# Optimization experiments

Hardware: AMD Instinct MI355X
Metric: run time of the kernel (lower is better)

The kernel has to match this reference:

```python
import jax, jax.numpy as jnp
import numpy as np

B_, N, C = 1024, 64, 512
H = 16          # num_heads
NW = 64         # number of windows (B_ % NW == 0)


def setup_inputs() -> dict:
    key = jax.random.key(0)
    ks = jax.random.split(key, 7)
    return {
        "x": jax.random.normal(ks[0], (B_, N, C), jnp.float32),
        "mask": jax.random.normal(ks[1], (NW, N, N), jnp.float32),
        "qkv_w": jax.random.normal(ks[2], (C, 3 * C), jnp.float32) * 0.02,
        "qkv_b": jax.random.normal(ks[3], (3 * C,), jnp.float32) * 0.02,
        "proj_w": jax.random.normal(ks[4], (C, C), jnp.float32) * 0.02,
        "proj_b": jax.random.normal(ks[5], (C,), jnp.float32) * 0.02,
        "bias_table": jax.random.normal(ks[6], (2 * N - 1, H), jnp.float32) * 0.02,
    }


def reference(x, mask, qkv_w, qkv_b, proj_w, proj_b, bias_table):
    b_, n, c = x.shape
    h = bias_table.shape[1]
    ws = (bias_table.shape[0] + 1) // 2  # window_size, == n here
    d = c // h
    scale = d ** -0.5

    qkv = x @ qkv_w + qkv_b                                   # [B_, N, 3C]
    qkv = qkv.reshape(b_, n, 3, h, d).transpose(2, 0, 3, 1, 4)  # [3, B_, H, N, d]
    q, k, v = qkv[0] * scale, qkv[1], qkv[2]

    attn = jnp.einsum('bhnd,bhmd->bhnm', q, k)                # [B_, H, N, N]

    coords = jnp.arange(ws)
    rel_idx = coords[:, None] - coords[None, :] + ws - 1       # [ws, ws]
    bias = bias_table[rel_idx].transpose(2, 0, 1)              # [H, ws, ws]
    attn = attn + bias[None]

    nw = mask.shape[0]
    attn = attn.reshape(b_ // nw, nw, h, n, n) + mask[None, :, None]
    attn = attn.reshape(-1, h, n, n)
    attn = jax.nn.softmax(attn, axis=-1)

    out = jnp.einsum('bhnm,bhmd->bhnd', attn, v)               # [B_, H, N, d]
    # Faithful to the TF code: v keeps a leading singleton dim after tf.split,
    # so attn@v is [1, B_, H, N, d]; perm [0,2,1,3,4] swaps B_ and H before
    # the final reshape to (B_, N, C).
    out = out[None].transpose(0, 2, 1, 3, 4).reshape(b_, n, c)
    return out @ proj_w + proj_b
```

## Files before the change

### kernel.cpp

```cpp
#include <hip/hip_runtime.h>
#include <hip/hip_bf16.h>
#include <stdint.h>

typedef __attribute__((ext_vector_type(4))) float f32x4;
typedef __attribute__((ext_vector_type(8))) short s16x8;

__device__ __forceinline__ short f2bf(float f) {
  union { float f; uint32_t u; } v; v.f = f;
  uint32_t r = v.u + 0x7FFFu + ((v.u >> 16) & 1u);
  return (short)(r >> 16);
}
__device__ __forceinline__ uint32_t pack2bf(float a, float b) {
  return (uint32_t)(uint16_t)f2bf(a) | ((uint32_t)(uint16_t)f2bf(b) << 16);
}

__device__ __forceinline__ void async16(const void* g, void* l) {
  __builtin_amdgcn_global_load_lds(
      (const __attribute__((address_space(1))) void*)g,
      (__attribute__((address_space(3))) void*)l, 16, 0, 0);
}

__global__ __launch_bounds__(256) void k_cast_bf16(const float* __restrict__ in,
                                                   short* __restrict__ out, int n8) {
  int i = blockIdx.x * 256 + threadIdx.x;
  if (i >= n8) return;
  const float4* p = (const float4*)in + (size_t)i * 2;
  float4 a = p[0], b = p[1];
  s16x8 o;
  o[0] = f2bf(a.x); o[1] = f2bf(a.y); o[2] = f2bf(a.z); o[3] = f2bf(a.w);
  o[4] = f2bf(b.x); o[5] = f2bf(b.y); o[6] = f2bf(b.z); o[7] = f2bf(b.w);
  ((s16x8*)out)[i] = o;
}

__global__ __launch_bounds__(256) void k_transpose_cast(const float* __restrict__ in,
                                                        short* __restrict__ out,
                                                        int K, int N) {
  __shared__ float tile[64][65];
  const int bx = blockIdx.x;
  const int by = blockIdx.y;
  const int tx = threadIdx.x & 63, ty = threadIdx.x >> 6;
#pragma unroll
  for (int r = ty; r < 64; r += 4)
    tile[r][tx] = in[(size_t)(by * 64 + r) * N + bx * 64 + tx];
  __syncthreads();
#pragma unroll
  for (int r = ty; r < 64; r += 4)
    out[(size_t)(bx * 64 + r) * K + by * 64 + tx] = f2bf(tile[tx][r]);
}

#define TILE_SH 16384

template <bool F32OUT, int NBN, int KK>
__global__ __launch_bounds__(512, 2) void k_gemm256p(const short* __restrict__ A,
                                                     const short* __restrict__ Bw,
                                                     const float* __restrict__ bias,
                                                     void* __restrict__ C,
                                                     int N, int nrounds) {
  __shared__ short lds[2 * 2 * TILE_SH];
  const int t = threadIdx.x;
  const int w = t >> 6, l = t & 63;
  const int wm = w >> 2, wn = w & 3;
  const int swz = (((int)blockIdx.x & 7) << 5) + ((int)blockIdx.x >> 3);

  const int NT = KK >> 6;
  const int NS = nrounds * NT;

  auto stage = [&](const short* __restrict__ G, int row0, int kt, short* dst) {
#pragma unroll
    for (int L = 0; L < 2; ++L) {
      int cw = L * 512 + (t & ~63);
      int c = cw + l;
      int r = c >> 3, s = c & 7;
      async16(G + (size_t)(row0 + r) * KK + kt + ((s ^ (r & 7)) << 3), dst + cw * 8);
    }
  };
  auto issueA = [&](int step, int bmv, int hf) {
    int kt = step & 7;
    stage(A, bmv * 256 + hf * 128, kt * 64, lds + (kt & 1) * 32768 + hf * 8192);
  };
  auto issueB = [&](int step, int bnv, int hf) {
    int kt = step & 7;
    stage(Bw, bnv * 256 + hf * 128, kt * 64, lds + (kt & 1) * 32768 + TILE_SH + hf * 8192);
  };

  const int g = l >> 4, v = l & 7;
  int ofsA[2], ofsB[2];
#pragma unroll
  for (int ks = 0; ks < 2; ++ks) {
    ofsA[ks] = (wm * 128 + (l & 15)) * 64 + (((ks * 4 + g) ^ v) << 3);
    ofsB[ks] = (wn * 64 + (l & 15)) * 64 + (((ks * 4 + g) ^ v) << 3);
  }

  f32x4 acc[8][4] = {};
  s16x8 bfr[4][2];

  {
    const int bm0 = swz / NBN, bn0 = swz % NBN;
    issueB(0, bn0, 0); issueB(0, bn0, 1);
    issueA(0, bm0, 0); issueA(0, bm0, 1);
    issueB(1, bn0, 0); issueB(1, bn0, 1);
  }
  asm volatile("s_waitcnt vmcnt(4)" ::: "memory");
  __builtin_amdgcn_s_barrier();

#define PHASE(AI0, STAGE_STMT, TAIL_STMT)                                                                      \
  {                                                                                                            \
    s16x8 a00 = *(const s16x8*)(Ab + ofsA[0] + (AI0) * 1024);                                                  \
    s16x8 a01 = *(const s16x8*)(Ab + ofsA[1] + (AI0) * 1024);                                                  \
    s16x8 a10 = *(const s16x8*)(Ab + ofsA[0] + ((AI0) + 1) * 1024);                                            \
    s16x8 a11 = *(const s16x8*)(Ab + ofsA[1] + ((AI0) + 1) * 1024);                                            \
    STAGE_STMT;                                                                                                \
    __builtin_amdgcn_s_barrier();                                                                              \
    asm volatile("s_waitcnt lgkmcnt(0)" ::: "memory");                                                         \
    __builtin_amdgcn_s_setprio(1);                                                                             \
    _Pragma("unroll")                                                                                          \
    for (int nj = 0; nj < 4; ++nj) {                                                                           \
      acc[(AI0)][nj] = __builtin_amdgcn_mfma_f32_16x16x32_bf16(a00, bfr[nj][0], acc[(AI0)][nj], 0, 0, 0);      \
      acc[(AI0)][nj] = __builtin_amdgcn_mfma_f32_16x16x32_bf16(a01, bfr[nj][1], acc[(AI0)][nj], 0, 0, 0);      \
      acc[(AI0) + 1][nj] = __builtin_amdgcn_mfma_f32_16x16x32_bf16(a10, bfr[nj][0], acc[(AI0) + 1][nj], 0, 0, 0); \
      acc[(AI0) + 1][nj] = __builtin_amdgcn_mfma_f32_16x16x32_bf16(a11, bfr[nj][1], acc[(AI0) + 1][nj], 0, 0, 0); \
    }                                                                                                          \
    __builtin_amdgcn_s_setprio(0);                                                                             \
    TAIL_STMT;                                                                                                 \
    __builtin_amdgcn_s_barrier();                                                                              \
  }

  for (int j = 0; j < nrounds; ++j) {
    const int tauc = swz + (j << 8);
    const int bmc = tauc / NBN, bnc = tauc % NBN;
    for (int T = 0; T < NT; ++T) {
      const int s = (j << 3) + T;
      const int s1 = s + 1, s2 = s + 2;
      const int tau1 = swz + (((s1) >> 3) << 8);
      const int tau2 = swz + (((s2) >> 3) << 8);
      const int bm1 = tau1 / NBN;
      const int bn2 = tau2 % NBN;
      const short* Ab = lds + (T & 1) * 32768;
      const short* Bb = Ab + TILE_SH;
#pragma unroll
      for (int nj = 0; nj < 4; ++nj)
#pragma unroll
        for (int ks = 0; ks < 2; ++ks)
          bfr[nj][ks] = *(const s16x8*)(Bb + ofsB[ks] + nj * 1024);

      PHASE(0, if (s1 < NS) issueA(s1, bm1, 0), );
      PHASE(2, if (s1 < NS) issueA(s1, bm1, 1), );
      PHASE(4, if (s2 < NS) issueB(s2, bn2, 0), );
      PHASE(6, if (s2 < NS) issueB(s2, bn2, 1),
            if (s2 < NS) { asm volatile("s_waitcnt vmcnt(4)" ::: "memory"); }
            else if (s1 < NS) { asm volatile("s_waitcnt vmcnt(0)" ::: "memory"); });
    }

#pragma unroll
    for (int ai = 0; ai < 8; ++ai)
#pragma unroll
      for (int nj = 0; nj < 4; ++nj) {
        int col = bnc * 256 + wn * 64 + nj * 16 + (l & 15);
        float bv = bias[col];
#pragma unroll
        for (int r = 0; r < 4; ++r) {
          int row = bmc * 256 + wm * 128 + ai * 16 + (l >> 4) * 4 + r;
          float vv = acc[ai][nj][r] + bv;
          if (F32OUT)
            ((float*)C)[(size_t)row * N + col] = vv;
          else
            ((short*)C)[(size_t)row * N + col] = f2bf(vv);
        }
      }
#pragma unroll
    for (int ai = 0; ai < 8; ++ai)
#pragma unroll
      for (int nj = 0; nj < 4; ++nj)
        acc[ai][nj] = (f32x4){0.f, 0.f, 0.f, 0.f};
  }
#undef PHASE
}

__global__ __launch_bounds__(256) void k_attn(const short* __restrict__ qkv,
                                              const float* __restrict__ mask,
                                              const float* __restrict__ bias_table,
                                              short* __restrict__ Y) {
  __shared__ float mask_lds[64 * 64];
  __shared__ float bias_lds[4][128];
  __shared__ short p_lds[4][64][72];
  __shared__ short v_lds[4][64][40];

  const int t = threadIdx.x, wv = t >> 6, ln = t & 63;
  const int b = blockIdx.x;
  const int h = blockIdx.y * 4 + wv;
  const int hi = ln >> 4, lo = ln & 15;

  const float4* mk = (const float4*)(mask + (size_t)(b & 63) * 4096);
#pragma unroll
  for (int u = 0; u < 4; ++u) {
    int idx = t + 256 * u;
    int row = idx >> 4, c4 = (idx & 15) * 4;
    *(float4*)&mask_lds[row * 64 + (c4 ^ ((row & 7) << 2))] = mk[idx];
  }
  for (int u = ln; u < 127; u += 64) bias_lds[wv][u] = bias_table[u * 16 + h];

  const short* qb = qkv + (size_t)b * 64 * 1536 + h * 32;
  const short* vg = qb + 1024;
#pragma unroll
  for (int u = 0; u < 4; ++u) {
    int row = u * 16 + (ln >> 2), c8 = (ln & 3) * 8;
    *(s16x8*)&v_lds[wv][row][c8] = *(const s16x8*)(vg + (size_t)row * 1536 + c8);
  }
  __syncthreads();

  s16x8 qf[4], kf[4];
#pragma unroll
  for (int i = 0; i < 4; ++i) {
    qf[i] = *(const s16x8*)(qb + (size_t)(16 * i + lo) * 1536 + hi * 8);
    kf[i] = *(const s16x8*)(qb + (size_t)(16 * i + lo) * 1536 + 512 + hi * 8);
  }
  f32x4 s2[4][4] = {};
#pragma unroll
  for (int j = 0; j < 4; ++j)
#pragma unroll
    for (int i = 0; i < 4; ++i)
      s2[j][i] = __builtin_amdgcn_mfma_f32_16x16x32_bf16(kf[j], qf[i], s2[j][i], 0, 0, 0);

  const float scale = 0.17677669529663687f;
#pragma unroll
  for (int i = 0; i < 4; ++i) {
    const int n = 16 * i + lo;
    const int msw = (n & 7) << 2;
    float x[16];
    float vmax = -1e30f;
#pragma unroll
    for (int j = 0; j < 4; ++j)
#pragma unroll
      for (int r = 0; r < 4; ++r) {
        int m = 16 * j + 4 * hi + r;
        float xx = s2[j][i][r] * scale + bias_lds[wv][n - m + 63] +
                   mask_lds[n * 64 + (m ^ msw)];
        x[j * 4 + r] = xx;
        vmax = fmaxf(vmax, xx);
      }
    vmax = fmaxf(vmax, __shfl_xor(vmax, 16, 64));
    vmax = fmaxf(vmax, __shfl_xor(vmax, 32, 64));
    float sum = 0.f;
#pragma unroll
    for (int u = 0; u < 16; ++u) {
      x[u] = __expf(x[u] - vmax);
      sum += x[u];
    }
    sum += __shfl_xor(sum, 16, 64);
    sum += __shfl_xor(sum, 32, 64);
    float rsv = 1.0f / sum;
#pragma unroll
    for (int j = 0; j < 4; ++j)
#pragma unroll
      for (int rp = 0; rp < 2; ++rp)
        *(uint32_t*)&p_lds[wv][n][16 * j + 4 * hi + rp * 2] =
            pack2bf(x[j * 4 + rp * 2] * rsv, x[j * 4 + rp * 2 + 1] * rsv);
  }

  f32x4 o2[2][4] = {};
#pragma unroll
  for (int kk = 0; kk < 2; ++kk) {
    s16x8 pa[4];
#pragma unroll
    for (int i2 = 0; i2 < 4; ++i2)
      pa[i2] = *(const s16x8*)&p_lds[wv][16 * i2 + lo][kk * 32 + hi * 8];
#pragma unroll
    for (int j2 = 0; j2 < 2; ++j2) {
      s16x8 vf;
#pragma unroll
      for (int jj = 0; jj < 8; ++jj)
        vf[jj] = v_lds[wv][kk * 32 + hi * 8 + jj][16 * j2 + lo];
#pragma unroll
      for (int i2 = 0; i2 < 4; ++i2)
        o2[j2][i2] = __builtin_amdgcn_mfma_f32_16x16x32_bf16(vf, pa[i2], o2[j2][i2], 0, 0, 0);
    }
  }

  const int rr = h * 64 + (b >> 4);
#pragma unroll
  for (int i2 = 0; i2 < 4; ++i2) {
    int ss = (b & 15) * 4 + i2;
    short* yr = Y + ((size_t)rr * 64 + ss) * 512 + lo * 32 + 4 * hi;
#pragma unroll
    for (int j2 = 0; j2 < 2; ++j2) {
      uint2 pk;
      pk.x = pack2bf(o2[j2][i2][0], o2[j2][i2][1]);
      pk.y = pack2bf(o2[j2][i2][2], o2[j2][i2][3]);
      *(uint2*)(yr + 16 * j2) = pk;
    }
  }
}

extern "C" void kernel_launch(void* const* d_in, const int* in_sizes, int n_in,
                              void* d_out, int out_size, void* d_ws, size_t ws_size,
                              hipStream_t stream) {
  const float* x      = (const float*)d_in[0];
  const float* mask   = (const float*)d_in[1];
  const float* qkv_w  = (const float*)d_in[2];
  const float* qkv_b  = (const float*)d_in[3];
  const float* proj_w = (const float*)d_in[4];
  const float* proj_b = (const float*)d_in[5];
  const float* btab   = (const float*)d_in[6];
  float* out = (float*)d_out;

  char* w = (char*)d_ws;
  short* qkv_ws = (short*)w;
  short* xbf    = (short*)(w + (size_t)65536 * 1536 * 2);
  short* Y      = xbf;
  short* wT     = (short*)(w + (size_t)65536 * 1536 * 2 + (size_t)65536 * 512 * 2);
  short* projT  = wT + 1536 * 512;

  k_cast_bf16<<<16384, 256, 0, stream>>>(x, xbf, 33554432 / 8);
  k_transpose_cast<<<dim3(24, 8), 256, 0, stream>>>(qkv_w, wT, 512, 1536);
  k_transpose_cast<<<dim3(8, 8), 256, 0, stream>>>(proj_w, projT, 512, 512);
  k_gemm256p<false, 6, 512><<<256, 512, 0, stream>>>(xbf, wT, qkv_b, qkv_ws, 1536, 6);
  k_attn<<<dim3(1024, 4), 256, 0, stream>>>(qkv_ws, mask, btab, Y);
  k_gemm256p<true, 2, 512><<<256, 512, 0, stream>>>(Y, projT, proj_b, out, 512, 2);
}
```

Baseline: 290.5 us.

## Fuse fp32-to-bf16 cast of x into QKV GEMM A-tile loading

Removes the separate cast kernel that converted x to bf16. The QKV GEMM now loads fp32 A tiles into registers, converts them and writes them to LDS with a swizzled layout, while B still uses async global-to-LDS loads. This saves one full read and write pass over the 128MB input. In exchange the A load moves through registers, which adds register pressure and synchronous LDS writes, and reads twice as many bytes of A per tile inside the GEMM, which may hurt pipelining.

```diff
diff --git a/kernel.cpp b/kernel.cpp
--- a/kernel.cpp
+++ b/kernel.cpp
@@ -18,18 +18,6 @@
   __builtin_amdgcn_global_load_lds(
       (const __attribute__((address_space(1))) void*)g,
       (__attribute__((address_space(3))) void*)l, 16, 0, 0);
-}
-
-__global__ __launch_bounds__(256) void k_cast_bf16(const float* __restrict__ in,
-                                                   short* __restrict__ out, int n8) {
-  int i = blockIdx.x * 256 + threadIdx.x;
-  if (i >= n8) return;
-  const float4* p = (const float4*)in + (size_t)i * 2;
-  float4 a = p[0], b = p[1];
-  s16x8 o;
-  o[0] = f2bf(a.x); o[1] = f2bf(a.y); o[2] = f2bf(a.z); o[3] = f2bf(a.w);
-  o[4] = f2bf(b.x); o[5] = f2bf(b.y); o[6] = f2bf(b.z); o[7] = f2bf(b.w);
-  ((s16x8*)out)[i] = o;
 }
 
 __global__ __launch_bounds__(256) void k_transpose_cast(const float* __restrict__ in,
@@ -50,12 +38,14 @@
 
 #define TILE_SH 16384
 
-template <bool F32OUT, int NBN, int KK>
-__global__ __launch_bounds__(512, 2) void k_gemm256p(const short* __restrict__ A,
+template <bool F32OUT, int NBN, bool AF32, int KK>
+__global__ __launch_bounds__(512, 2) void k_gemm256p(const void* __restrict__ Av,
                                                      const short* __restrict__ Bw,
                                                      const float* __restrict__ bias,
                                                      void* __restrict__ C,
                                                      int N, int nrounds) {
+  const short* A  = (const short*)Av;
+  const float* Af = (const float*)Av;
   __shared__ short lds[2 * 2 * TILE_SH];
   const int t = threadIdx.x;
   const int w = t >> 6, l = t & 63;
@@ -83,6 +73,35 @@
     stage(Bw, bnv * 256 + hf * 128, kt * 64, lds + (kt & 1) * 32768 + TILE_SH + hf * 8192);
   };
 
+  float4 fa[4][2];
+  auto loadA = [&](int step, int bmv) {
+    int kt = step & 7;
+#pragma unroll
+    for (int q = 0; q < 4; ++q) {
+      int hf = q >> 1;
+      int cc = (q & 1) * 512 + (t & ~63) + l;
+      int r = hf * 128 + (cc >> 3), sc = cc & 7;
+      const float* src = Af + (size_t)(bmv * 256 + r) * KK + kt * 64 + ((sc ^ (r & 7)) << 3);
+      fa[q][0] = *(const float4*)src;
+      fa[q][1] = *(const float4*)(src + 4);
+    }
+  };
+  auto writeA = [&](int step) {
+    int kt = step & 7;
+    short* base = lds + (kt & 1) * 32768;
+#pragma unroll
+    for (int q = 0; q < 4; ++q) {
+      int hf = q >> 1;
+      int cc = (q & 1) * 512 + (t & ~63) + l;
+      int4 o;
+      o.x = (int)pack2bf(fa[q][0].x, fa[q][0].y);
+      o.y = (int)pack2bf(fa[q][0].z, fa[q][0].w);
+      o.z = (int)pack2bf(fa[q][1].x, fa[q][1].y);
+      o.w = (int)pack2bf(fa[q][1].z, fa[q][1].w);
+      *(int4*)(base + hf * 8192 + (size_t)cc * 8) = o;
+    }
+  };
+
   const int g = l >> 4, v = l & 7;
   int ofsA[2], ofsB[2];
 #pragma unroll
@@ -96,12 +115,34 @@
 
   {
     const int bm0 = swz / NBN, bn0 = swz % NBN;
-    issueB(0, bn0, 0); issueB(0, bn0, 1);
-    issueA(0, bm0, 0); issueA(0, bm0, 1);
-    issueB(1, bn0, 0); issueB(1, bn0, 1);
-  }
-  asm volatile("s_waitcnt vmcnt(4)" ::: "memory");
+    if (AF32) {
+      loadA(0, bm0);
+      issueB(0, bn0, 0); issueB(0, bn0, 1);
+      issueB(1, bn0, 0); issueB(1, bn0, 1);
+      asm volatile("s_waitcnt vmcnt(4)" ::: "memory");
+      writeA(0);
+      asm volatile("s_waitcnt lgkmcnt(0)" ::: "memory");
+    } else {
+      issueB(0, bn0, 0); issueB(0, bn0, 1);
+      issueA(0, bm0, 0); issueA(0, bm0, 1);
+      issueB(1, bn0, 0); issueB(1, bn0, 1);
+      asm volatile("s_waitcnt vmcnt(4)" ::: "memory");
+    }
+  }
   __builtin_amdgcn_s_barrier();
+
+  auto tailStd = [&](int s1v, int s2v) {
+    if (s2v < NS) { asm volatile("s_waitcnt vmcnt(4)" ::: "memory"); }
+    else if (s1v < NS) { asm volatile("s_waitcnt vmcnt(0)" ::: "memory"); }
+  };
+  auto tailF32 = [&](int s1v, int s2v) {
+    if (s2v < NS) { asm volatile("s_waitcnt vmcnt(4)" ::: "memory"); }
+    else if (s1v < NS) { asm volatile("s_waitcnt vmcnt(0)" ::: "memory"); }
+    if (s1v < NS) {
+      writeA(s1v);
+      asm volatile("s_waitcnt lgkmcnt(0)" ::: "memory");
+    }
+  };
 
 #define PHASE(AI0, STAGE_STMT, TAIL_STMT)                                                                      \
   {                                                                                                            \
@@ -143,12 +184,17 @@
         for (int ks = 0; ks < 2; ++ks)
           bfr[nj][ks] = *(const s16x8*)(Bb + ofsB[ks] + nj * 1024);
 
-      PHASE(0, if (s1 < NS) issueA(s1, bm1, 0), );
-      PHASE(2, if (s1 < NS) issueA(s1, bm1, 1), );
-      PHASE(4, if (s2 < NS) issueB(s2, bn2, 0), );
-      PHASE(6, if (s2 < NS) issueB(s2, bn2, 1),
-            if (s2 < NS) { asm volatile("s_waitcnt vmcnt(4)" ::: "memory"); }
-            else if (s1 < NS) { asm volatile("s_waitcnt vmcnt(0)" ::: "memory"); });
+      if (AF32) {
+        PHASE(0, if (s1 < NS) loadA(s1, bm1), );
+        PHASE(2, , );
+        PHASE(4, if (s2 < NS) issueB(s2, bn2, 0), );
+        PHASE(6, if (s2 < NS) issueB(s2, bn2, 1), tailF32(s1, s2));
+      } else {
+        PHASE(0, if (s1 < NS) issueA(s1, bm1, 0), );
+        PHASE(2, if (s1 < NS) issueA(s1, bm1, 1), );
+        PHASE(4, if (s2 < NS) issueB(s2, bn2, 0), );
+        PHASE(6, if (s2 < NS) issueB(s2, bn2, 1), tailStd(s1, s2));
+      }
     }
 
 #pragma unroll
@@ -305,15 +351,13 @@
 
   char* w = (char*)d_ws;
   short* qkv_ws = (short*)w;
-  short* xbf    = (short*)(w + (size_t)65536 * 1536 * 2);
-  short* Y      = xbf;
+  short* Y      = (short*)(w + (size_t)65536 * 1536 * 2);
   short* wT     = (short*)(w + (size_t)65536 * 1536 * 2 + (size_t)65536 * 512 * 2);
   short* projT  = wT + 1536 * 512;
 
-  k_cast_bf16<<<16384, 256, 0, stream>>>(x, xbf, 33554432 / 8);
   k_transpose_cast<<<dim3(24, 8), 256, 0, stream>>>(qkv_w, wT, 512, 1536);
   k_transpose_cast<<<dim3(8, 8), 256, 0, stream>>>(proj_w, projT, 512, 512);
-  k_gemm256p<false, 6, 512><<<256, 512, 0, stream>>>(xbf, wT, qkv_b, qkv_ws, 1536, 6);
+  k_gemm256p<false, 6, true, 512><<<256, 512, 0, stream>>>(x, wT, qkv_b, qkv_ws, 1536, 6);
   k_attn<<<dim3(1024, 4), 256, 0, stream>>>(qkv_ws, mask, btab, Y);
-  k_gemm256p<true, 2, 512><<<256, 512, 0, stream>>>(Y, projT, proj_b, out, 512, 2);
-}
+  k_gemm256p<true, 2, false, 512><<<256, 512, 0, stream>>>(Y, projT, proj_b, out, 512, 2);
+}
```

New measurement: 404.0 us. +39.0%, slower.
